# Performance work log

Hardware: AMD Instinct MI355X
Metric: run time of the kernel (lower is better)

The kernel has to match this reference:

```python
import jax, jax.numpy as jnp
import numpy as np

N, E, D_IN, H = 40000, 640000, 128, 128
R, B = 8, 30  # num_relations = 2*n_speakers**2, num_bases


def setup_inputs() -> dict:
    key = jax.random.key(0)
    ks = jax.random.split(key, 10)
    node_features = jax.random.normal(ks[0], (N, D_IN), jnp.float32)
    edge_index = jax.random.randint(ks[1], (2, E), 0, N)
    edge_type = jax.random.randint(ks[2], (E,), 0, R)
    edge_norm = jax.random.uniform(ks[3], (E,), jnp.float32)
    s_in = 1.0 / np.sqrt(D_IN)
    s_h = 1.0 / np.sqrt(H)
    basis = jax.random.normal(ks[4], (B, D_IN, H), jnp.float32) * s_in
    comp = jax.random.normal(ks[5], (R, B), jnp.float32) * (1.0 / np.sqrt(B))
    root = jax.random.normal(ks[6], (D_IN, H), jnp.float32) * s_in
    bias1 = jnp.zeros((H,), jnp.float32)
    w_rel = jax.random.normal(ks[7], (H, H), jnp.float32) * s_h
    w_root2 = jax.random.normal(ks[8], (H, H), jnp.float32) * s_h
    bias2 = jnp.zeros((H,), jnp.float32)
    return dict(node_features=node_features, edge_index=edge_index,
                edge_norm=edge_norm, edge_type=edge_type,
                basis=basis, comp=comp, root=root, bias1=bias1,
                w_rel=w_rel, w_root2=w_root2, bias2=bias2)


def reference(node_features, edge_index, edge_norm, edge_type,
              basis, comp, root, bias1, w_rel, w_root2, bias2):
    n = node_features.shape[0]
    src, dst = edge_index[0], edge_index[1]  # messages flow src -> dst

    # ---- RGCNConv (basis decomposition, mean aggregation, root + bias) ----
    # Per-relation weights from bases: [R, D_in, H]
    w = jnp.einsum('rb,bio->rio', comp, basis)
    # Transform all nodes by every relation once (avoids per-edge matmul): [R, N, H]
    xw = jnp.einsum('nd,rdo->rno', node_features, w)
    msgs = xw[edge_type, src]                                  # [E, H]
    agg = jax.ops.segment_sum(msgs, dst, num_segments=n)       # [N, H]
    deg = jax.ops.segment_sum(jnp.ones_like(dst, dtype=node_features.dtype),
                              dst, num_segments=n)
    agg = agg / jnp.maximum(deg, 1.0)[:, None]                 # mean aggregation
    h = agg + node_features @ root + bias1                     # [N, H]

    # ---- GraphConv (add aggregation): W_rel * sum_j x_j + W_root * x_i + b ----
    nbr = jax.ops.segment_sum(h[src], dst, num_segments=n)     # [N, H]
    out = nbr @ w_rel + h @ w_root2 + bias2
    return out
```

## Files before the change

### kernel.cpp

```cpp
#include <hip/hip_runtime.h>
#include <stdint.h>

#define DH 128
#define NB 30
#define NR 8

typedef short bf16x8 __attribute__((ext_vector_type(8)));
typedef float f32x4 __attribute__((ext_vector_type(4)));
typedef float f32x2 __attribute__((ext_vector_type(2)));

static __device__ __forceinline__ unsigned short f2bf(float f) {
    unsigned u = __float_as_uint(f);
    u += 0x7fffu + ((u >> 16) & 1u);
    return (unsigned short)(u >> 16);
}
static __device__ __forceinline__ float bflo(unsigned u) { return __uint_as_float(u << 16); }
static __device__ __forceinline__ float bfhi(unsigned u) { return __uint_as_float(u & 0xffff0000u); }

__global__ __launch_bounds__(256) void k_prephist(const float* __restrict__ comp,
                                                  const float* __restrict__ basis,
                                                  const float* __restrict__ root,
                                                  const float* __restrict__ wrel,
                                                  const float* __restrict__ wroot2,
                                                  unsigned short* __restrict__ wallT,
                                                  unsigned short* __restrict__ WT2,
                                                  const int* __restrict__ dstA, int E,
                                                  int* __restrict__ deg, int histB) {
    int b = blockIdx.x;
    int tid = threadIdx.x;
    if (b < histB) {
        int e = b * 256 + tid;
        if (e < E) atomicAdd(&deg[dstA[e]], 1);
        return;
    }
    int unit = (b - histB) * 2 + (tid >> 7);
    int o = tid & 127;
    int i = unit & 127;
    int y = unit >> 7;
    if (y < NR) {
        float s = 0.f;
        #pragma unroll
        for (int bb = 0; bb < NB; ++bb)
            s += comp[y * NB + bb] * basis[((size_t)bb * DH + i) * DH + o];
        wallT[((size_t)y * DH + o) * DH + i] = f2bf(s);
    } else if (y == NR) {
        wallT[((size_t)NR * DH + o) * DH + i] = f2bf(root[i * DH + o]);
    } else {
        const float* W = (y == NR + 2) ? wroot2 : wrel;
        WT2[((size_t)(y - NR - 1) * DH + o) * DH + i] = f2bf(W[i * DH + o]);
    }
}

__global__ __launch_bounds__(1024) void k_scan(const int* __restrict__ deg, int n, int total_n,
                                               int* __restrict__ offsets,
                                               unsigned long long* __restrict__ st,
                                               int* __restrict__ ticket) {
    __shared__ int s[1024];
    __shared__ int bid_s, pre_s;
    const int tid = threadIdx.x;
    if (tid == 0) bid_s = atomicAdd(ticket, 1);
    __syncthreads();
    const int b = bid_s;
    int i = b * 1024 + tid;
    int v = (i < n) ? deg[i] : 0;
    s[tid] = v;
    __syncthreads();
    for (int off = 1; off < 1024; off <<= 1) {
        int t = (tid >= off) ? s[tid - off] : 0;
        __syncthreads();
        s[tid] += t;
        __syncthreads();
    }
    if (tid == 0) {
        int total = s[1023];
        atomicExch(&st[b], (1ULL << 62) | (unsigned long long)(unsigned)total);
        long long pre = 0;
        int t = b - 1;
        while (t >= 0) {
            unsigned long long w;
            do { w = atomicAdd(&st[t], 0ULL); } while (w == 0ULL);
            pre += (long long)(w & 0x3FFFFFFFFFFFFFFFULL);
            if ((w >> 62) == 2ULL) break;
            --t;
        }
        atomicExch(&st[b], (2ULL << 62) | (unsigned long long)(pre + total));
        pre_s = (int)pre;
    }
    __syncthreads();
    if (i < total_n) offsets[i] = pre_s + s[tid] - v;
}

__global__ void k_scatter(const int* __restrict__ src, const int* __restrict__ dstA,
                          const int* __restrict__ etype, int E,
                          const int* __restrict__ offsets, int* __restrict__ cursor,
                          unsigned* __restrict__ sorted) {
    int e = blockIdx.x * blockDim.x + threadIdx.x;
    if (e >= E) return;
    int d = dstA[e];
    int pos = offsets[d] + atomicAdd(&cursor[d], 1);
    sorted[pos] = (unsigned)src[e] | ((unsigned)etype[e] << 17);
}

__global__ __launch_bounds__(256) void k_gemm1m(const float* __restrict__ x,
                                                const unsigned short* __restrict__ wallT,
                                                const float* __restrict__ bias1,
                                                int Nn,
                                                unsigned* __restrict__ xw8,
                                                unsigned short* __restrict__ hb) {
    __shared__ __align__(16) unsigned short As[128][136];
    __shared__ __align__(16) unsigned short Bs[128][136];
    const int tid = threadIdx.x;
    const int wave = tid >> 6, lane = tid & 63;
    const int g = blockIdx.y;
    const int rowbase = blockIdx.x * 128;
    const int lq = lane >> 4, lr = lane & 15;

    #pragma unroll
    for (int it = 0; it < 8; ++it) {
        int c = it * 256 + tid;
        int row = c >> 4, col = c & 15;
        int rg = rowbase + row; if (rg >= Nn) rg = Nn - 1;
        float4 v0 = *(const float4*)&x[(size_t)rg * DH + col * 8];
        float4 v1 = *(const float4*)&x[(size_t)rg * DH + col * 8 + 4];
        uint4 u;
        u.x = (unsigned)f2bf(v0.x) | ((unsigned)f2bf(v0.y) << 16);
        u.y = (unsigned)f2bf(v0.z) | ((unsigned)f2bf(v0.w) << 16);
        u.z = (unsigned)f2bf(v1.x) | ((unsigned)f2bf(v1.y) << 16);
        u.w = (unsigned)f2bf(v1.z) | ((unsigned)f2bf(v1.w) << 16);
        *(uint4*)&As[row][col * 8] = u;
    }

    for (int rr = 0; rr < 3; ++rr) {
        const int r = g * 3 + rr;
        const unsigned short* WT = wallT + (size_t)r * DH * DH;
        if (rr) __syncthreads();
        #pragma unroll
        for (int it = 0; it < 8; ++it) {
            int c = it * 256 + tid;
            int row = c >> 4, col = c & 15;
            *(uint4*)&Bs[row][col * 8] = *(const uint4*)&WT[(size_t)row * DH + col * 8];
        }
        __syncthreads();

        f32x4 acc[2][8];
        #pragma unroll
        for (int mt = 0; mt < 2; ++mt)
            #pragma unroll
            for (int nt = 0; nt < 8; ++nt) acc[mt][nt] = (f32x4)0.f;

        #pragma unroll
        for (int ks = 0; ks < 4; ++ks) {
            const int ko = ks * 32 + lq * 8;
            bf16x8 a0 = *(const bf16x8*)&As[wave * 32 + lr][ko];
            bf16x8 a1 = *(const bf16x8*)&As[wave * 32 + 16 + lr][ko];
            #pragma unroll
            for (int nt = 0; nt < 8; ++nt) {
                bf16x8 b = *(const bf16x8*)&Bs[nt * 16 + lr][ko];
                acc[0][nt] = __builtin_amdgcn_mfma_f32_16x16x32_bf16(a0, b, acc[0][nt], 0, 0, 0);
                acc[1][nt] = __builtin_amdgcn_mfma_f32_16x16x32_bf16(a1, b, acc[1][nt], 0, 0, 0);
            }
        }
        __syncthreads();

        float bv[8];
        #pragma unroll
        for (int nt = 0; nt < 8; ++nt) bv[nt] = (r == NR) ? bias1[nt * 16 + lr] : 0.f;
        #pragma unroll
        for (int mt = 0; mt < 2; ++mt)
            #pragma unroll
            for (int nt = 0; nt < 8; ++nt)
                #pragma unroll
                for (int reg = 0; reg < 4; ++reg) {
                    int ml = wave * 32 + mt * 16 + lq * 4 + reg;
                    Bs[ml][nt * 16 + lr] = f2bf(acc[mt][nt][reg] + bv[nt]);
                }
        __syncthreads();

        if (r < NR) {
            unsigned* dst = xw8 + ((size_t)r * Nn + rowbase) * (DH / 4);
            #pragma unroll
            for (int it = 0; it < 8; ++it) {
                int c = it * 256 + tid;
                int row = c >> 4, col = c & 15;
                if (rowbase + row < Nn) {
                    uint4 q = *(uint4*)&Bs[row][col * 8];
                    uint2 o;
                    o.x = __builtin_amdgcn_cvt_pk_fp8_f32(bflo(q.x), bfhi(q.x), 0, false);
                    o.x = __builtin_amdgcn_cvt_pk_fp8_f32(bflo(q.y), bfhi(q.y), o.x, true);
                    o.y = __builtin_amdgcn_cvt_pk_fp8_f32(bflo(q.z), bfhi(q.z), 0, false);
                    o.y = __builtin_amdgcn_cvt_pk_fp8_f32(bflo(q.w), bfhi(q.w), o.y, true);
                    *(uint2*)&dst[(size_t)row * (DH / 4) + col * 2] = o;
                }
            }
        } else {
            #pragma unroll
            for (int it = 0; it < 8; ++it) {
                int c = it * 256 + tid;
                int row = c >> 4, col = c & 15;
                if (rowbase + row < Nn)
                    *(uint4*)&hb[((size_t)(rowbase + row)) * DH + col * 8] = *(uint4*)&Bs[row][col * 8];
            }
        }
    }
}

__global__ __launch_bounds__(256) void k_agg1(const int* __restrict__ offsets,
                                              const unsigned* __restrict__ sorted,
                                              const unsigned* __restrict__ xw8,
                                              const unsigned* __restrict__ hb32,
                                              int Nn, unsigned* __restrict__ hbf) {
    int w = (blockIdx.x * blockDim.x + threadIdx.x) >> 6;
    if (w >= Nn) return;
    int lane = threadIdx.x & 63;
    int half = lane >> 5, sub = lane & 31;
    int s = offsets[w], e = offsets[w + 1];
    float a0 = 0.f, a1 = 0.f, a2 = 0.f, a3 = 0.f;
    int p = s;
    for (; p + 16 <= e; p += 16) {
        unsigned pk[8];
        #pragma unroll
        for (int j = 0; j < 8; ++j) pk[j] = sorted[p + 2 * j + half];
        unsigned u[8];
        #pragma unroll
        for (int j = 0; j < 8; ++j)
            u[j] = xw8[((size_t)(pk[j] >> 17) * Nn + (pk[j] & 0x1FFFFu)) * 32 + sub];
        #pragma unroll
        for (int j = 0; j < 8; ++j) {
            f32x2 lo = __builtin_amdgcn_cvt_pk_f32_fp8(u[j], false);
            f32x2 hi = __builtin_amdgcn_cvt_pk_f32_fp8(u[j], true);
            a0 += lo.x; a1 += lo.y; a2 += hi.x; a3 += hi.y;
        }
    }
    if (p < e) {
        unsigned pk[8]; float m[8];
        #pragma unroll
        for (int j = 0; j < 8; ++j) {
            int q = p + 2 * j + half; bool v = q < e;
            pk[j] = sorted[v ? q : e - 1];
            m[j] = v ? 1.f : 0.f;
        }
        unsigned u[8];
        #pragma unroll
        for (int j = 0; j < 8; ++j)
            u[j] = xw8[((size_t)(pk[j] >> 17) * Nn + (pk[j] & 0x1FFFFu)) * 32 + sub];
        #pragma unroll
        for (int j = 0; j < 8; ++j) {
            f32x2 lo = __builtin_amdgcn_cvt_pk_f32_fp8(u[j], false);
            f32x2 hi = __builtin_amdgcn_cvt_pk_f32_fp8(u[j], true);
            a0 = fmaf(m[j], lo.x, a0);
            a1 = fmaf(m[j], lo.y, a1);
            a2 = fmaf(m[j], hi.x, a2);
            a3 = fmaf(m[j], hi.y, a3);
        }
    }
    a0 += __shfl_xor(a0, 32, 64);
    a1 += __shfl_xor(a1, 32, 64);
    a2 += __shfl_xor(a2, 32, 64);
    a3 += __shfl_xor(a3, 32, 64);
    if (half == 0) {
        float invd = 1.0f / fmaxf((float)(e - s), 1.0f);
        uint2 hv = *(const uint2*)&hb32[(size_t)w * 64 + sub * 2];
        float h0 = bflo(hv.x) + a0 * invd;
        float h1 = bfhi(hv.x) + a1 * invd;
        float h2 = bflo(hv.y) + a2 * invd;
        float h3 = bfhi(hv.y) + a3 * invd;
        uint2 o;
        o.x = (unsigned)f2bf(h0) | ((unsigned)f2bf(h1) << 16);
        o.y = (unsigned)f2bf(h2) | ((unsigned)f2bf(h3) << 16);
        *(uint2*)&hbf[(size_t)w * 64 + sub * 2] = o;
    }
}

__global__ __launch_bounds__(256) void k_agg2(const int* __restrict__ offsets,
                                              const unsigned* __restrict__ sorted,
                                              const uint2* __restrict__ hbf2,
                                              int Nn, uint2* __restrict__ nbr2) {
    int w = (blockIdx.x * blockDim.x + threadIdx.x) >> 6;
    if (w >= Nn) return;
    int lane = threadIdx.x & 63;
    int half = lane >> 5, sub = lane & 31;
    int s = offsets[w], e = offsets[w + 1];
    float a0 = 0.f, a1 = 0.f, a2 = 0.f, a3 = 0.f;
    int p = s;
    for (; p + 16 <= e; p += 16) {
        unsigned pk[8];
        #pragma unroll
        for (int j = 0; j < 8; ++j) pk[j] = sorted[p + 2 * j + half];
        uint2 u[8];
        #pragma unroll
        for (int j = 0; j < 8; ++j)
            u[j] = hbf2[(size_t)(pk[j] & 0x1FFFFu) * 32 + sub];
        #pragma unroll
        for (int j = 0; j < 8; ++j) {
            a0 += bflo(u[j].x); a1 += bfhi(u[j].x);
            a2 += bflo(u[j].y); a3 += bfhi(u[j].y);
        }
    }
    if (p < e) {
        unsigned pk[8]; float m[8];
        #pragma unroll
        for (int j = 0; j < 8; ++j) {
            int q = p + 2 * j + half; bool v = q < e;
            pk[j] = sorted[v ? q : e - 1];
            m[j] = v ? 1.f : 0.f;
        }
        uint2 u[8];
        #pragma unroll
        for (int j = 0; j < 8; ++j)
            u[j] = hbf2[(size_t)(pk[j] & 0x1FFFFu) * 32 + sub];
        #pragma unroll
        for (int j = 0; j < 8; ++j) {
            a0 = fmaf(m[j], bflo(u[j].x), a0);
            a1 = fmaf(m[j], bfhi(u[j].x), a1);
            a2 = fmaf(m[j], bflo(u[j].y), a2);
            a3 = fmaf(m[j], bfhi(u[j].y), a3);
        }
    }
    a0 += __shfl_xor(a0, 32, 64);
    a1 += __shfl_xor(a1, 32, 64);
    a2 += __shfl_xor(a2, 32, 64);
    a3 += __shfl_xor(a3, 32, 64);
    if (half == 0) {
        uint2 o;
        o.x = (unsigned)f2bf(a0) | ((unsigned)f2bf(a1) << 16);
        o.y = (unsigned)f2bf(a2) | ((unsigned)f2bf(a3) << 16);
        nbr2[(size_t)w * 32 + sub] = o;
    }
}

__global__ __launch_bounds__(256) void k_gemm2m(const unsigned short* __restrict__ nbrbf,
                                                const unsigned short* __restrict__ hbf,
                                                const unsigned short* __restrict__ WT2,
                                                const float* __restrict__ bias2,
                                                int Nn, float* __restrict__ out) {
    __shared__ __align__(16) unsigned short As[128][136];
    __shared__ __align__(16) unsigned short Bs[128][136];
    const int tid = threadIdx.x;
    const int wave = tid >> 6, lane = tid & 63;
    const int rowbase = blockIdx.x * 128;
    const int lq = lane >> 4, lr = lane & 15;

    f32x4 acc[2][8];
    #pragma unroll
    for (int mt = 0; mt < 2; ++mt)
        #pragma unroll
        for (int nt = 0; nt < 8; ++nt) acc[mt][nt] = (f32x4)0.f;

    for (int ph = 0; ph < 2; ++ph) {
        const unsigned short* A = ph ? hbf : nbrbf;
        const unsigned short* WT = WT2 + (size_t)ph * DH * DH;
        if (ph) __syncthreads();
        #pragma unroll
        for (int it = 0; it < 8; ++it) {
            int c = it * 256 + tid;
            int row = c >> 4, col = c & 15;
            int rg = rowbase + row; if (rg >= Nn) rg = Nn - 1;
            *(uint4*)&As[row][col * 8] = *(const uint4*)&A[(size_t)rg * DH + col * 8];
            *(uint4*)&Bs[row][col * 8] = *(const uint4*)&WT[(size_t)row * DH + col * 8];
        }
        __syncthreads();
        #pragma unroll
        for (int ks = 0; ks < 4; ++ks) {
            const int ko = ks * 32 + lq * 8;
            bf16x8 a0 = *(const bf16x8*)&As[wave * 32 + lr][ko];
            bf16x8 a1 = *(const bf16x8*)&As[wave * 32 + 16 + lr][ko];
            #pragma unroll
            for (int nt = 0; nt < 8; ++nt) {
                bf16x8 b = *(const bf16x8*)&Bs[nt * 16 + lr][ko];
                acc[0][nt] = __builtin_amdgcn_mfma_f32_16x16x32_bf16(a0, b, acc[0][nt], 0, 0, 0);
                acc[1][nt] = __builtin_amdgcn_mfma_f32_16x16x32_bf16(a1, b, acc[1][nt], 0, 0, 0);
            }
        }
    }

    float bv[8];
    #pragma unroll
    for (int nt = 0; nt < 8; ++nt) bv[nt] = bias2[nt * 16 + lr];
    #pragma unroll
    for (int mt = 0; mt < 2; ++mt)
        #pragma unroll
        for (int nt = 0; nt < 8; ++nt)
            #pragma unroll
            for (int reg = 0; reg < 4; ++reg) {
                int m = rowbase + wave * 32 + mt * 16 + lq * 4 + reg;
                if (m < Nn) out[(size_t)m * DH + nt * 16 + lr] = acc[mt][nt][reg] + bv[nt];
            }
}

extern "C" void kernel_launch(void* const* d_in, const int* in_sizes, int n_in,
                              void* d_out, int out_size, void* d_ws, size_t ws_size,
                              hipStream_t stream) {
    const float* x      = (const float*)d_in[0];
    const int*   eidx   = (const int*)d_in[1];
    const int*   etype  = (const int*)d_in[3];
    const float* basis  = (const float*)d_in[4];
    const float* comp   = (const float*)d_in[5];
    const float* root   = (const float*)d_in[6];
    const float* bias1  = (const float*)d_in[7];
    const float* wrel   = (const float*)d_in[8];
    const float* wroot2 = (const float*)d_in[9];
    const float* bias2  = (const float*)d_in[10];
    float* out = (float*)d_out;

    const int N = in_sizes[0] / DH;
    const int E = in_sizes[3];
    const int* srcA = eidx;
    const int* dstA = eidx + E;

    char* ws = (char*)d_ws;
    size_t off = 0;
    auto alloc = [&](size_t bytes) -> void* {
        void* p = (void*)(ws + off);
        off += (bytes + 255) & ~(size_t)255;
        return p;
    };
    int* deg           = (int*)alloc((size_t)N * 4);
    int* cursor        = (int*)alloc((size_t)N * 4);
    unsigned long long* st = (unsigned long long*)alloc(64 * 8);
    int* ticket        = (int*)alloc(256);
    int* offsets       = (int*)alloc((size_t)(N + 1) * 4);
    unsigned* sorted   = (unsigned*)alloc((size_t)E * 4);
    unsigned short* wallT = (unsigned short*)alloc((size_t)(NR + 1) * DH * DH * 2);
    unsigned short* WT2   = (unsigned short*)alloc((size_t)2 * DH * DH * 2);
    unsigned* xw8      = (unsigned*)alloc((size_t)NR * N * DH);
    unsigned short* hb = (unsigned short*)alloc((size_t)N * DH * 2);
    unsigned* hbf      = (unsigned*)alloc((size_t)N * (DH / 2) * 4);
    unsigned* nbrbf    = (unsigned*)alloc((size_t)N * (DH / 2) * 4);
    (void)ws_size; (void)n_in; (void)out_size;

    hipMemsetAsync(deg, 0, (size_t)N * 8 + 768, stream);

    const int histB = (E + 255) / 256;
    k_prephist<<<histB + 704, 256, 0, stream>>>(comp, basis, root, wrel, wroot2,
                                                wallT, WT2, dstA, E, deg, histB);

    const int totn = N + 1;
    const int nsb = (totn + 1023) / 1024;
    k_scan<<<nsb, 1024, 0, stream>>>(deg, N, totn, offsets, st, ticket);
    k_scatter<<<(E + 255) / 256, 256, 0, stream>>>(srcA, dstA, etype, E, offsets, cursor, sorted);

    const int gx = (N + 127) / 128;
    k_gemm1m<<<dim3(gx, 3), 256, 0, stream>>>(x, wallT, bias1, N, xw8, hb);
    k_agg1<<<(N * 64) / 256, 256, 0, stream>>>(offsets, sorted, xw8,
                                               (const unsigned*)hb, N, hbf);
    k_agg2<<<(N * 64) / 256, 256, 0, stream>>>(offsets, sorted, (const uint2*)hbf, N, (uint2*)nbrbf);
    k_gemm2m<<<gx, 256, 0, stream>>>((const unsigned short*)nbrbf, (const unsigned short*)hbf,
                                     WT2, bias2, N, out);
}
```

Measured before the change: 243.2 us.

## Fuse edge scatter into GEMM1 launch and seed cursor from scan

Edge bucketing by destination now runs in extra blocks appended to the first GEMM launch, so the scatter overlaps with the matrix multiply and one kernel launch is removed. The scan kernel now writes the exclusive offsets directly into the cursor array, so the scatter only does an atomicAdd on the cursor and no longer reads offsets. This also shrinks the memset, since cursor is no longer zeroed. The trade-off is that the scatter blocks compete with the GEMM blocks for CUs, and the GEMM grid changes from 2D to a 1D index computation.

```diff
diff --git a/kernel.cpp b/kernel.cpp
--- a/kernel.cpp
+++ b/kernel.cpp
@@ -53,6 +53,7 @@
 
 __global__ __launch_bounds__(1024) void k_scan(const int* __restrict__ deg, int n, int total_n,
                                                int* __restrict__ offsets,
+                                               int* __restrict__ cursor,
                                                unsigned long long* __restrict__ st,
                                                int* __restrict__ ticket) {
     __shared__ int s[1024];
@@ -87,32 +88,41 @@
         pre_s = (int)pre;
     }
     __syncthreads();
-    if (i < total_n) offsets[i] = pre_s + s[tid] - v;
-}
-
-__global__ void k_scatter(const int* __restrict__ src, const int* __restrict__ dstA,
-                          const int* __restrict__ etype, int E,
-                          const int* __restrict__ offsets, int* __restrict__ cursor,
-                          unsigned* __restrict__ sorted) {
-    int e = blockIdx.x * blockDim.x + threadIdx.x;
-    if (e >= E) return;
-    int d = dstA[e];
-    int pos = offsets[d] + atomicAdd(&cursor[d], 1);
-    sorted[pos] = (unsigned)src[e] | ((unsigned)etype[e] << 17);
-}
-
-__global__ __launch_bounds__(256) void k_gemm1m(const float* __restrict__ x,
+    int ov = pre_s + s[tid] - v;
+    if (i < total_n) offsets[i] = ov;
+    if (i < n) cursor[i] = ov;
+}
+
+__global__ __launch_bounds__(256) void k_gemm1s(const float* __restrict__ x,
                                                 const unsigned short* __restrict__ wallT,
                                                 const float* __restrict__ bias1,
                                                 int Nn,
                                                 unsigned* __restrict__ xw8,
-                                                unsigned short* __restrict__ hb) {
+                                                unsigned short* __restrict__ hb,
+                                                const int* __restrict__ src,
+                                                const int* __restrict__ dstA,
+                                                const int* __restrict__ etype, int E,
+                                                int* __restrict__ cursor,
+                                                unsigned* __restrict__ sorted,
+                                                int gemmB, int gx) {
     __shared__ __align__(16) unsigned short As[128][136];
     __shared__ __align__(16) unsigned short Bs[128][136];
     const int tid = threadIdx.x;
+    const int b = blockIdx.x;
+
+    if (b >= gemmB) {
+        const int stride = (gridDim.x - gemmB) * 256;
+        for (int e = (b - gemmB) * 256 + tid; e < E; e += stride) {
+            int d = dstA[e];
+            int pos = atomicAdd(&cursor[d], 1);
+            sorted[pos] = (unsigned)src[e] | ((unsigned)etype[e] << 17);
+        }
+        return;
+    }
+
     const int wave = tid >> 6, lane = tid & 63;
-    const int g = blockIdx.y;
-    const int rowbase = blockIdx.x * 128;
+    const int g = b / gx;
+    const int rowbase = (b % gx) * 128;
     const int lq = lane >> 4, lr = lane & 15;
 
     #pragma unroll
@@ -155,9 +165,9 @@
             bf16x8 a1 = *(const bf16x8*)&As[wave * 32 + 16 + lr][ko];
             #pragma unroll
             for (int nt = 0; nt < 8; ++nt) {
-                bf16x8 b = *(const bf16x8*)&Bs[nt * 16 + lr][ko];
-                acc[0][nt] = __builtin_amdgcn_mfma_f32_16x16x32_bf16(a0, b, acc[0][nt], 0, 0, 0);
-                acc[1][nt] = __builtin_amdgcn_mfma_f32_16x16x32_bf16(a1, b, acc[1][nt], 0, 0, 0);
+                bf16x8 bb = *(const bf16x8*)&Bs[nt * 16 + lr][ko];
+                acc[0][nt] = __builtin_amdgcn_mfma_f32_16x16x32_bf16(a0, bb, acc[0][nt], 0, 0, 0);
+                acc[1][nt] = __builtin_amdgcn_mfma_f32_16x16x32_bf16(a1, bb, acc[1][nt], 0, 0, 0);
             }
         }
         __syncthreads();
@@ -415,9 +425,9 @@
         return p;
     };
     int* deg           = (int*)alloc((size_t)N * 4);
-    int* cursor        = (int*)alloc((size_t)N * 4);
     unsigned long long* st = (unsigned long long*)alloc(64 * 8);
     int* ticket        = (int*)alloc(256);
+    int* cursor        = (int*)alloc((size_t)N * 4);
     int* offsets       = (int*)alloc((size_t)(N + 1) * 4);
     unsigned* sorted   = (unsigned*)alloc((size_t)E * 4);
     unsigned short* wallT = (unsigned short*)alloc((size_t)(NR + 1) * DH * DH * 2);
@@ -428,7 +438,7 @@
     unsigned* nbrbf    = (unsigned*)alloc((size_t)N * (DH / 2) * 4);
     (void)ws_size; (void)n_in; (void)out_size;
 
-    hipMemsetAsync(deg, 0, (size_t)N * 8 + 768, stream);
+    hipMemsetAsync(deg, 0, (size_t)N * 4 + 768, stream);
 
     const int histB = (E + 255) / 256;
     k_prephist<<<histB + 704, 256, 0, stream>>>(comp, basis, root, wrel, wroot2,
@@ -436,11 +446,15 @@
 
     const int totn = N + 1;
     const int nsb = (totn + 1023) / 1024;
-    k_scan<<<nsb, 1024, 0, stream>>>(deg, N, totn, offsets, st, ticket);
-    k_scatter<<<(E + 255) / 256, 256, 0, stream>>>(srcA, dstA, etype, E, offsets, cursor, sorted);
+    k_scan<<<nsb, 1024, 0, stream>>>(deg, N, totn, offsets, cursor, st, ticket);
 
     const int gx = (N + 127) / 128;
-    k_gemm1m<<<dim3(gx, 3), 256, 0, stream>>>(x, wallT, bias1, N, xw8, hb);
+    const int gemmB = gx * 3;
+    const int scatB = 1280;
+    k_gemm1s<<<gemmB + scatB, 256, 0, stream>>>(x, wallT, bias1, N, xw8, hb,
+                                                srcA, dstA, etype, E, cursor, sorted,
+                                                gemmB, gx);
+
     k_agg1<<<(N * 64) / 256, 256, 0, stream>>>(offsets, sorted, xw8,
                                                (const unsigned*)hb, N, hbf);
     k_agg2<<<(N * 64) / 256, 256, 0, stream>>>(offsets, sorted, (const uint2*)hbf, N, (uint2*)nbrbf);
```

New measurement: 241.1 us. Within noise of the previous version (-0.9%).
